# Performance work log

Measured on AMD Instinct MI355X. Metric: run time of the kernel, lower is better.

Reference implementation:

```python
import jax, jax.numpy as jnp
import numpy as np

NUM_EMBEDDINGS = 8192
EMA_DECAY = 0.99


def setup_inputs() -> dict:
    key = jax.random.key(0)
    k1, k2 = jax.random.split(key)
    encodings = jax.random.normal(k1, (16, 128, 32, 32), dtype=jnp.float32)
    weight = 0.02 * jax.random.normal(k2, (NUM_EMBEDDINGS, 128), dtype=jnp.float32)
    return {"encodings": encodings, "weight": weight}


def reference(encodings, weight):
    B, C, H, W = encodings.shape
    K = weight.shape[0]
    # [B, C, H, W] -> [N, C], N = B*H*W
    x = encodings.transpose(0, 2, 3, 1).reshape(-1, C)
    # pairwise squared distances via norms + matmul: [N, K]
    dist = (
        jnp.sum(x * x, axis=1, keepdims=True)
        + jnp.sum(weight * weight, axis=1)[None, :]
        - 2.0 * jnp.matmul(x, weight.T)
    )
    quantized_ids = jnp.argmin(dist, axis=1)  # [N] int
    # straight-through estimator
    q = x + jax.lax.stop_gradient(weight[quantized_ids] - x)  # [N, C]
    # training-mode EMA codebook update (scatter-add counts and sums)
    counts = jax.ops.segment_sum(
        jnp.ones((x.shape[0],), dtype=x.dtype), quantized_ids, num_segments=K
    )
    sums = jax.ops.segment_sum(x, quantized_ids, num_segments=K)
    new_means = sums / (counts[:, None] + 1e-12)
    new_weight = EMA_DECAY * weight + (1.0 - EMA_DECAY) * new_means
    ids_out = quantized_ids.reshape(B, H, W)
    q_out = q.reshape(B, H, W, C).transpose(0, 3, 1, 2)  # [B, C, H, W]
    return ids_out, q_out, new_weight
```

## Files before the change

### kernel.cpp

```cpp
#include <hip/hip_runtime.h>
#include <stdint.h>
#include <stddef.h>


#define N_ROWS   16384
#define K_CODES  8192
#define C_DIM    128
#define ITEMS_CAP 32768u

typedef _Float16 f16x8 __attribute__((ext_vector_type(8)));
typedef float    f32x4 __attribute__((ext_vector_type(4)));

__global__ __launch_bounds__(256) void prep(const float* __restrict__ enc,
                                            const float* __restrict__ w,
                                            _Float16* __restrict__ Ap,
                                            _Float16* __restrict__ Bp,
                                            float* __restrict__ xT,
                                            float* __restrict__ xnorm,
                                            float* __restrict__ wnorm,
                                            float* __restrict__ wnmax128) {
  __shared__ float t[128][65];
  const int tid = threadIdx.x;
  if (blockIdx.x < 256) {
    const int b = blockIdx.x >> 4;
    const int hw0 = (blockIdx.x & 15) << 6;
    #pragma unroll
    for (int i = 0; i < 32; ++i) {
      int idx = i * 256 + tid;
      int c = idx >> 6, hwl = idx & 63;
      t[c][hwl] = enc[((size_t)(b * 128 + c) << 10) + hw0 + hwl];
    }
    __syncthreads();
    const int r = tid >> 2, sub = tid & 3;
    const int n = (b << 10) + hw0 + r;
    const int R = n >> 4, m = n & 15;
    float s = 0.f;
    #pragma unroll
    for (int q = 0; q < 4; ++q) {
      f16x8 hv;
      float vv[8];
      #pragma unroll
      for (int e = 0; e < 8; ++e) {
        float v = t[sub * 32 + q * 8 + e][r];
        vv[e] = v;
        s += v * v;
        hv[e] = (_Float16)v;
      }
      *(f16x8*)(Ap + ((size_t)(R * 4 + sub) * 64 + (m + 16 * q)) * 8) = hv;
      *(float4*)(xT + (size_t)n * 128 + sub * 32 + q * 8) =
          (float4){vv[0], vv[1], vv[2], vv[3]};
      *(float4*)(xT + (size_t)n * 128 + sub * 32 + q * 8 + 4) =
          (float4){vv[4], vv[5], vv[6], vv[7]};
    }
    s += __shfl_xor(s, 1);
    s += __shfl_xor(s, 2);
    if (sub == 0) xnorm[n] = s;
  } else {
    __shared__ float wred[4];
    const int kk = (blockIdx.x - 256) * 64 + (tid >> 2), sub = tid & 3;
    const int R = kk >> 4, m = kk & 15;
    const float* base = w + (size_t)kk * C_DIM + sub * 32;
    float s = 0.f;
    #pragma unroll
    for (int q = 0; q < 4; ++q) {
      f16x8 hv;
      float4 va = *(const float4*)(base + q * 8);
      float4 vb = *(const float4*)(base + q * 8 + 4);
      float vv[8] = {va.x, va.y, va.z, va.w, vb.x, vb.y, vb.z, vb.w};
      #pragma unroll
      for (int e = 0; e < 8; ++e) { s += vv[e] * vv[e]; hv[e] = (_Float16)vv[e]; }
      *(f16x8*)(Bp + ((size_t)(R * 4 + sub) * 64 + (m + 16 * q)) * 8) = hv;
    }
    s += __shfl_xor(s, 1);
    s += __shfl_xor(s, 2);
    if (sub == 0) wnorm[kk] = s;
    float wx = s;
    #pragma unroll
    for (int st = 1; st <= 32; st <<= 1) wx = fmaxf(wx, __shfl_xor(wx, st));
    if ((tid & 63) == 0) wred[tid >> 6] = wx;
    __syncthreads();
    if (tid == 0)
      wnmax128[blockIdx.x - 256] =
          fmaxf(fmaxf(wred[0], wred[1]), fmaxf(wred[2], wred[3]));
  }
}

__global__ __launch_bounds__(512) void gemm_argmin(
    const _Float16* __restrict__ Ap, const _Float16* __restrict__ Bp,
    const float* __restrict__ wnorm,
    float* __restrict__ pd1h, unsigned short* __restrict__ pd2h,
    unsigned* __restrict__ icount, unsigned* __restrict__ hcount)
{
  __shared__ _Float16 sbuf[2][8192];
  const int tid = threadIdx.x;
  const int lane = tid & 63, wave = tid >> 6;
  const int m = lane & 15, q = lane >> 4;
  const int cs = blockIdx.x;
  const int row0 = blockIdx.y * 128;
  const int Tr = blockIdx.y * 8 + wave;

  if (cs == 0 && blockIdx.y == 0 && tid == 0) {
    *icount = 0u; *hcount = 0u;
  }

#define STAGE(b, hgn) do {                                                   \
    const size_t bh_ = ((size_t)((cs * 64 + (hgn) * 4) * 4) << 9);           \
    _Pragma("unroll")                                                        \
    for (int r_ = 0; r_ < 2; ++r_) {                                         \
      __builtin_amdgcn_global_load_lds(                                      \
          (const __attribute__((address_space(1))) void*)                    \
              (Bp + bh_ + ((size_t)(r_ * 512 + tid) << 3)),                  \
          (__attribute__((address_space(3))) void*)                          \
              (&sbuf[b][(r_ * 512 + tid) << 3]),                             \
          16, 0, 0);                                                         \
    }                                                                        \
  } while (0)

  f16x8 bx[4];
  #pragma unroll
  for (int kc = 0; kc < 4; ++kc)
    bx[kc] = *(const f16x8*)(Ap + (((size_t)Tr * 4 + kc) << 9) + (lane << 3));
  const int row = row0 + wave * 16 + m;
  const unsigned q2 = (unsigned)(q << 2);

  STAGE(0, 0);

  for (int hg = 0; hg < 16; ++hg) {
    __syncthreads();
    if (hg < 15) STAGE((hg + 1) & 1, hg + 1);
    const _Float16* fb = &sbuf[hg & 1][0];
    f32x4 acc[4];
    #pragma unroll
    for (int t = 0; t < 4; ++t) acc[t] = (f32x4){0.f, 0.f, 0.f, 0.f};
    #pragma unroll
    for (int kc = 0; kc < 4; ++kc) {
      #pragma unroll
      for (int t = 0; t < 4; ++t) {
        f16x8 a = *(const f16x8*)(fb + ((t * 4 + kc) << 9) + (lane << 3));
        acc[t] = __builtin_amdgcn_mfma_f32_16x16x32_f16(a, bx[kc], acc[t], 0, 0, 0);
      }
    }
    float m1t[4], m2t[4];
    #pragma unroll
    for (int t = 0; t < 4; ++t) {
      const int cb = (cs * 64 + hg * 4 + t) * 16 + 4 * q;
      float4 wnq = *(const float4*)(wnorm + cb);
      const unsigned e0 = (unsigned)(t << 4);
      unsigned b0 = (__float_as_uint(fmaf(-2.0f, acc[t][0], wnq.x)) & 0xFFFFFFC0u) | e0;
      unsigned b1 = (__float_as_uint(fmaf(-2.0f, acc[t][1], wnq.y)) & 0xFFFFFFC0u) | (e0 | 1u);
      unsigned b2 = (__float_as_uint(fmaf(-2.0f, acc[t][2], wnq.z)) & 0xFFFFFFC0u) | (e0 | 2u);
      unsigned b3 = (__float_as_uint(fmaf(-2.0f, acc[t][3], wnq.w)) & 0xFFFFFFC0u) | (e0 | 3u);
      float v0 = __uint_as_float(b0);
      float v1 = __uint_as_float(b1);
      float v2 = __uint_as_float(b2);
      float v3 = __uint_as_float(b3);
      float l1 = fminf(v0, v1), h1 = fmaxf(v0, v1);
      float l2 = fminf(v2, v3), h2 = fmaxf(v2, v3);
      m1t[t] = fminf(l1, l2);
      m2t[t] = fminf(fminf(h1, h2), fmaxf(l1, l2));
    }
    m2t[0] = fminf(fminf(m2t[0], m2t[1]), fmaxf(m1t[0], m1t[1]));
    m1t[0] = fminf(m1t[0], m1t[1]);
    m2t[2] = fminf(fminf(m2t[2], m2t[3]), fmaxf(m1t[2], m1t[3]));
    m1t[2] = fminf(m1t[2], m1t[3]);
    m2t[0] = fminf(fminf(m2t[0], m2t[2]), fmaxf(m1t[0], m1t[2]));
    m1t[0] = fminf(m1t[0], m1t[2]);
    float d1 = __uint_as_float(__float_as_uint(m1t[0]) | q2);
    float d2 = __uint_as_float(__float_as_uint(m2t[0]) | q2);
    #pragma unroll
    for (int s = 16; s <= 32; s <<= 1) {
      float o1 = __shfl_xor(d1, s), o2 = __shfl_xor(d2, s);
      d2 = fminf(fminf(d2, o2), fmaxf(d1, o1));
      d1 = fminf(d1, o1);
    }
    if (q == 0) {
      const int h = cs * 16 + hg;
      pd1h[(size_t)h * N_ROWS + row] = d1;
      unsigned bb = __float_as_uint(d2);
      bb += ((unsigned)((int)bb >> 31)) & 0xFFFFu;
      pd2h[(size_t)h * N_ROWS + row] = (unsigned short)(bb >> 16);
    }
  }
#undef STAGE
}

__global__ __launch_bounds__(256) void classify(
    const float* __restrict__ pd1h, const unsigned short* __restrict__ pd2h,
    const float* __restrict__ xnorm, const float* __restrict__ wnmax128,
    int* __restrict__ ids, unsigned* __restrict__ items,
    unsigned* __restrict__ icount, unsigned* __restrict__ hlist,
    unsigned* __restrict__ hcount, unsigned long long* __restrict__ keys,
    unsigned* __restrict__ cnt)
{
  __shared__ float wred[4];
  const int tid = threadIdx.x;
  const int gidx = blockIdx.x * 256 + tid;
  const int row = gidx >> 2, p = gidx & 3;
  if (p == 0) keys[row] = ~0ull;
  if (gidx < K_CODES) cnt[gidx] = 0u;
  float wv = wnmax128[tid & 127];
  #pragma unroll
  for (int st = 1; st <= 32; st <<= 1) wv = fmaxf(wv, __shfl_xor(wv, st));
  if ((tid & 63) == 0) wred[tid >> 6] = wv;
  __syncthreads();
  const float wm = fmaxf(fmaxf(wred[0], wred[1]), fmaxf(wred[2], wred[3]));

  float v1[32];
  float lmin = __builtin_inff();
  #pragma unroll
  for (int j = 0; j < 32; ++j) {
    v1[j] = pd1h[(size_t)(p * 32 + j) * N_ROWS + row];
    lmin = fminf(lmin, v1[j]);
  }
  lmin = fminf(lmin, __shfl_xor(lmin, 1));
  lmin = fminf(lmin, __shfl_xor(lmin, 2));
  float twoE = 2.0f * (0.0029297f * sqrtf(xnorm[row] * wm) + 5e-4f);
  float T = lmin + twoE;
  int nc = 0, hr = 0;
  unsigned cands[6];
  #pragma unroll 8
  for (int j = 0; j < 32; ++j) {
    const int h = p * 32 + j;
    float p2 = __uint_as_float(
        (unsigned)pd2h[(size_t)h * N_ROWS + row] << 16);
    if (p2 <= T) {
      unsigned hi = atomicAdd(hcount, 1u);
      hlist[hi] = ((unsigned)row << 7) | (unsigned)h;
      hr++;
    } else if (v1[j] <= T) {
      if (nc < 6) {
        cands[nc++] = (unsigned)h * 64u + (__float_as_uint(v1[j]) & 63u);
      } else {
        unsigned hi = atomicAdd(hcount, 1u);
        hlist[hi] = ((unsigned)row << 7) | (unsigned)h;
        hr++;
      }
    }
  }
  int nct = nc + __shfl_xor(nc, 1); nct += __shfl_xor(nct, 2);
  int hrt = hr + __shfl_xor(hr, 1); hrt += __shfl_xor(hrt, 2);
  if (hrt == 0 && nct == 1) {
    if (nc == 1) ids[row] = (int)cands[0];
  } else if (nc > 0) {
    unsigned base = atomicAdd(icount, (unsigned)nc);
    if (base + (unsigned)nc <= ITEMS_CAP) {
      for (int i2 = 0; i2 < nc; ++i2)
        items[base + i2] = ((unsigned)row << 13) | cands[i2];
    } else {
      for (int i2 = 0; i2 < nc; ++i2) {
        unsigned hi = atomicAdd(hcount, 1u);
        hlist[hi] = ((unsigned)row << 7) | (cands[i2] >> 6);
      }
    }
  }
}

__global__ __launch_bounds__(256) void refine(
    const float* __restrict__ xT, const float* __restrict__ w,
    const float* __restrict__ xnorm, const float* __restrict__ wnorm,
    const unsigned* __restrict__ items, const unsigned* __restrict__ icount,
    const unsigned* __restrict__ hlist, const unsigned* __restrict__ hcount,
    unsigned long long* __restrict__ keys) {
  const int tid = threadIdx.x;
  const int lane = tid & 63, wave = tid >> 6;
  const unsigned ic = *icount;
  const unsigned ica = ic <= ITEMS_CAP ? ic : ITEMS_CAP;
  for (unsigned i = blockIdx.x * 256 + tid; i < ica; i += gridDim.x * 256) {
    unsigned it = items[i];
    int row = (int)(it >> 13), c = (int)(it & 8191u);
    const float* xb = xT + (size_t)row * C_DIM;
    const float* wk = w + (size_t)c * C_DIM;
    float s = 0.f;
    #pragma unroll 8
    for (int c4 = 0; c4 < 32; ++c4) {
      float4 xv = *(const float4*)(xb + c4 * 4);
      float4 wv = *(const float4*)(wk + c4 * 4);
      s = fmaf(xv.x, wv.x, s);
      s = fmaf(xv.y, wv.y, s);
      s = fmaf(xv.z, wv.z, s);
      s = fmaf(xv.w, wv.w, s);
    }
    float d = (xnorm[row] + wnorm[c]) - 2.0f * s;
    unsigned sb = __float_as_uint(d);
    sb = (sb >> 31) ? ~sb : (sb | 0x80000000u);
    unsigned long long key = ((unsigned long long)sb << 32) | (unsigned)c;
    atomicMin(&keys[row], key);
  }
  __shared__ __align__(16) float xs[128];
  __shared__ unsigned long long red[4];
  const unsigned hc = *hcount;
  for (unsigned item = blockIdx.x; item < hc; item += gridDim.x) {
    const unsigned e = hlist[item];
    const int row = (int)(e >> 7), h = (int)(e & 127u);
    if (tid < 128)
      xs[tid] = xT[(size_t)row * C_DIM + tid];
    __syncthreads();
    const int code = h * 64 + (tid >> 2);
    const int qt = tid & 3;
    const float* wk = w + (size_t)code * C_DIM + qt * 32;
    float s = 0.f;
    #pragma unroll
    for (int c4 = 0; c4 < 8; ++c4) {
      float4 wv = *(const float4*)(wk + c4 * 4);
      float4 xv = *(const float4*)(&xs[qt * 32 + c4 * 4]);
      s = fmaf(xv.x, wv.x, s);
      s = fmaf(xv.y, wv.y, s);
      s = fmaf(xv.z, wv.z, s);
      s = fmaf(xv.w, wv.w, s);
    }
    s += __shfl_xor(s, 1);
    s += __shfl_xor(s, 2);
    unsigned long long best = ~0ull;
    if (qt == 0) {
      float d = (xnorm[row] + wnorm[code]) - 2.0f * s;
      unsigned sb = __float_as_uint(d);
      sb = (sb >> 31) ? ~sb : (sb | 0x80000000u);
      best = ((unsigned long long)sb << 32) | (unsigned)code;
    }
    #pragma unroll
    for (int st = 1; st <= 32; st <<= 1) {
      unsigned long long ok = __shfl_xor(best, st);
      best = ok < best ? ok : best;
    }
    if (lane == 0) red[wave] = best;
    __syncthreads();
    if (tid == 0) {
      unsigned long long bk = red[0];
      #pragma unroll
      for (int wv = 1; wv < 4; ++wv) bk = red[wv] < bk ? red[wv] : bk;
      atomicMin(&keys[row], bk);
    }
    __syncthreads();
  }
}

__global__ void resolve_ids(const unsigned long long* __restrict__ keys,
                            int* __restrict__ ids, unsigned* __restrict__ cnt,
                            float* __restrict__ out_ids) {
  int row = blockIdx.x * 256 + threadIdx.x;
  unsigned long long k = keys[row];
  int id = (k != ~0ull) ? (int)(unsigned)(k & 0xffffffffu) : ids[row];
  ids[row] = id;
  out_ids[row] = (float)id;
  atomicAdd(&cnt[id], 1u);
}

__global__ __launch_bounds__(256) void scan_offsets(
    const unsigned* __restrict__ cnt,
    unsigned* __restrict__ offs, unsigned* __restrict__ cursor) {
  __shared__ unsigned tot[256];
  const int tid = threadIdx.x;
  unsigned local[32], run = 0;
  #pragma unroll
  for (int i = 0; i < 32; ++i) { local[i] = run; run += cnt[tid * 32 + i]; }
  tot[tid] = run;
  __syncthreads();
  for (int st = 1; st < 256; st <<= 1) {
    unsigned v = (tid >= st) ? tot[tid - st] : 0u;
    __syncthreads();
    tot[tid] += v;
    __syncthreads();
  }
  unsigned excl = (tid == 0) ? 0u : tot[tid - 1];
  #pragma unroll
  for (int i = 0; i < 32; ++i) {
    unsigned o = excl + local[i];
    offs[tid * 32 + i] = o;
    cursor[tid * 32 + i] = o;
  }
}

__global__ void fill_rowlist(const int* __restrict__ ids,
                             unsigned* __restrict__ cursor,
                             int* __restrict__ rowlist) {
  int row = blockIdx.x * 256 + threadIdx.x;
  unsigned slot = atomicAdd(&cursor[ids[row]], 1u);
  rowlist[slot] = row;
}

__global__ __launch_bounds__(256) void qsum_final(
    const float* __restrict__ enc, const float* __restrict__ w,
    const int* __restrict__ ids,
    const unsigned* __restrict__ cnt, const unsigned* __restrict__ offs,
    const int* __restrict__ rowlist, const float* __restrict__ xT,
    float* __restrict__ outq, float* __restrict__ outw) {
  if (blockIdx.x < 2048) {
    int e = blockIdx.x * 1024 + threadIdx.x * 4;
    int c = (e >> 10) & 127;
    int b = e >> 17;
    int n = (b << 10) | (e & 1023);
    float4 x = *(const float4*)(enc + e);
    float4 o;
    o.x = x.x + (w[(size_t)ids[n + 0] * C_DIM + c] - x.x);
    o.y = x.y + (w[(size_t)ids[n + 1] * C_DIM + c] - x.y);
    o.z = x.z + (w[(size_t)ids[n + 2] * C_DIM + c] - x.z);
    o.w = x.w + (w[(size_t)ids[n + 3] * C_DIM + c] - x.w);
    *(float4*)(outq + e) = o;
  } else {
    const int tid = threadIdx.x;
    const int lane = tid & 63, wave = tid >> 6;
    const int k = (int)(blockIdx.x - 2048) * 4 + wave;
    const unsigned n0 = offs[k], nk = cnt[k];
    float S0a = 0.f, S0b = 0.f, S0c = 0.f, S0d = 0.f;
    float S1a = 0.f, S1b = 0.f, S1c = 0.f, S1d = 0.f;
    unsigned i = 0;
    for (; i + 4 <= nk; i += 4) {
      int r0 = rowlist[n0 + i],     r1 = rowlist[n0 + i + 1];
      int r2 = rowlist[n0 + i + 2], r3 = rowlist[n0 + i + 3];
      S0a += xT[(size_t)r0 * 128 + lane];      S1a += xT[(size_t)r0 * 128 + lane + 64];
      S0b += xT[(size_t)r1 * 128 + lane];      S1b += xT[(size_t)r1 * 128 + lane + 64];
      S0c += xT[(size_t)r2 * 128 + lane];      S1c += xT[(size_t)r2 * 128 + lane + 64];
      S0d += xT[(size_t)r3 * 128 + lane];      S1d += xT[(size_t)r3 * 128 + lane + 64];
    }
    for (; i < nk; ++i) {
      int r = rowlist[n0 + i];
      S0a += xT[(size_t)r * 128 + lane];
      S1a += xT[(size_t)r * 128 + lane + 64];
    }
    float S0 = (S0a + S0b) + (S0c + S0d);
    float S1 = (S1a + S1b) + (S1c + S1d);
    const float omd = (float)(1.0 - 0.99);
    float cf = (float)nk + 1e-12f;
    outw[(size_t)k * 128 + lane]      = 0.99f * w[(size_t)k * 128 + lane]      + omd * (S0 / cf);
    outw[(size_t)k * 128 + lane + 64] = 0.99f * w[(size_t)k * 128 + lane + 64] + omd * (S1 / cf);
  }
}

extern "C" void kernel_launch(void* const* d_in, const int* in_sizes, int n_in,
                              void* d_out, int out_size, void* d_ws, size_t ws_size,
                              hipStream_t stream) {
  const float* enc = (const float*)d_in[0];
  const float* w   = (const float*)d_in[1];
  float* out = (float*)d_out;
  float* out_ids = out;
  float* out_q   = out + N_ROWS;
  float* out_w   = out + N_ROWS + N_ROWS * C_DIM;

  char* ws = (char*)d_ws;
  _Float16* Ap  = (_Float16*)(ws);
  _Float16* Bp  = (_Float16*)(ws + 4194304);
  float* xnorm  = (float*)(ws + 6291456);
  float* wnorm  = (float*)(ws + 6356992);
  float* pd1h   = (float*)(ws + 6389760);
  unsigned short* pd2h = (unsigned short*)(ws + 14778368);
  float* wnmax128 = (float*)(ws + 18972672);
  int* ids      = (int*)(ws + 18973184);
  unsigned* hlist = (unsigned*)(ws + 19038720);
  unsigned* items = (unsigned*)(ws + 19563008);
  unsigned* icount = (unsigned*)(ws + 19694080);
  unsigned* hcount = (unsigned*)(ws + 19694084);
  unsigned* cnt    = (unsigned*)(ws + 19694096);
  unsigned* offs   = (unsigned*)(ws + 19726864);
  unsigned* cursor = (unsigned*)(ws + 19759632);
  unsigned long long* keys = (unsigned long long*)(ws + 19792400);
  int* rowlist  = (int*)(ws + 19923472);
  float* xT     = (float*)(ws + 20447248);
  (void)in_sizes; (void)n_in; (void)out_size; (void)ws_size;


  prep<<<384, 256, 0, stream>>>(enc, w, Ap, Bp, xT, xnorm, wnorm, wnmax128);
  gemm_argmin<<<dim3(8, N_ROWS / 128), 512, 0, stream>>>(
      Ap, Bp, wnorm, pd1h, pd2h, icount, hcount);
  classify<<<N_ROWS * 4 / 256, 256, 0, stream>>>(
      pd1h, pd2h, xnorm, wnmax128, ids, items, icount, hlist, hcount,
      keys, cnt);
  refine<<<2048, 256, 0, stream>>>(xT, w, xnorm, wnorm, items, icount,
                                   hlist, hcount, keys);
  resolve_ids<<<N_ROWS / 256, 256, 0, stream>>>(keys, ids, cnt, out_ids);
  scan_offsets<<<1, 256, 0, stream>>>(cnt, offs, cursor);
  fill_rowlist<<<N_ROWS / 256, 256, 0, stream>>>(ids, cursor, rowlist);
  qsum_final<<<2048 + K_CODES / 4, 256, 0, stream>>>(
      enc, w, ids, cnt, offs, rowlist, xT, out_q, out_w);
}
```

Measured before the change: 187.5 us.

## Replace counting-sort segment sum with float atomic scatter-add into codebook sums

Drops the scan_offsets and fill_rowlist kernels and the rowlist gather. Per-code sums are now built by float atomicAdd of each row's vector into a sums buffer, which refine zeroes and which reuses the pd2h workspace region. This removes two launches, a single-block scan and the serial gather loops, at the cost of many global float atomics that can contend on popular codes. Summation order becomes nondeterministic.

```diff
diff --git a/kernel.cpp b/kernel.cpp
--- a/kernel.cpp
+++ b/kernel.cpp
@@ -260,9 +260,11 @@
     const float* __restrict__ xnorm, const float* __restrict__ wnorm,
     const unsigned* __restrict__ items, const unsigned* __restrict__ icount,
     const unsigned* __restrict__ hlist, const unsigned* __restrict__ hcount,
-    unsigned long long* __restrict__ keys) {
+    unsigned long long* __restrict__ keys, float* __restrict__ sums) {
   const int tid = threadIdx.x;
   const int lane = tid & 63, wave = tid >> 6;
+  *(float2*)(sums + ((size_t)(blockIdx.x * 256 + tid) << 1)) =
+      (float2){0.f, 0.f};
   const unsigned ic = *icount;
   const unsigned ica = ic <= ITEMS_CAP ? ic : ITEMS_CAP;
   for (unsigned i = blockIdx.x * 256 + tid; i < ica; i += gridDim.x * 256) {
@@ -334,55 +336,36 @@
   }
 }
 
-__global__ void resolve_ids(const unsigned long long* __restrict__ keys,
-                            int* __restrict__ ids, unsigned* __restrict__ cnt,
-                            float* __restrict__ out_ids) {
-  int row = blockIdx.x * 256 + threadIdx.x;
+__global__ __launch_bounds__(256) void resolve_scatter(
+    const unsigned long long* __restrict__ keys,
+    int* __restrict__ ids, unsigned* __restrict__ cnt,
+    float* __restrict__ out_ids, const float* __restrict__ xT,
+    float* __restrict__ sums) {
+  const int gidx = blockIdx.x * 256 + threadIdx.x;
+  const int row = gidx >> 2, p = gidx & 3;
   unsigned long long k = keys[row];
   int id = (k != ~0ull) ? (int)(unsigned)(k & 0xffffffffu) : ids[row];
-  ids[row] = id;
-  out_ids[row] = (float)id;
-  atomicAdd(&cnt[id], 1u);
-}
-
-__global__ __launch_bounds__(256) void scan_offsets(
-    const unsigned* __restrict__ cnt,
-    unsigned* __restrict__ offs, unsigned* __restrict__ cursor) {
-  __shared__ unsigned tot[256];
-  const int tid = threadIdx.x;
-  unsigned local[32], run = 0;
+  if (p == 0) {
+    ids[row] = id;
+    out_ids[row] = (float)id;
+    atomicAdd(&cnt[id], 1u);
+  }
+  const float* xr = xT + (size_t)row * C_DIM + p * 32;
+  float* sr = sums + (size_t)id * C_DIM + p * 32;
   #pragma unroll
-  for (int i = 0; i < 32; ++i) { local[i] = run; run += cnt[tid * 32 + i]; }
-  tot[tid] = run;
-  __syncthreads();
-  for (int st = 1; st < 256; st <<= 1) {
-    unsigned v = (tid >= st) ? tot[tid - st] : 0u;
-    __syncthreads();
-    tot[tid] += v;
-    __syncthreads();
-  }
-  unsigned excl = (tid == 0) ? 0u : tot[tid - 1];
-  #pragma unroll
-  for (int i = 0; i < 32; ++i) {
-    unsigned o = excl + local[i];
-    offs[tid * 32 + i] = o;
-    cursor[tid * 32 + i] = o;
-  }
-}
-
-__global__ void fill_rowlist(const int* __restrict__ ids,
-                             unsigned* __restrict__ cursor,
-                             int* __restrict__ rowlist) {
-  int row = blockIdx.x * 256 + threadIdx.x;
-  unsigned slot = atomicAdd(&cursor[ids[row]], 1u);
-  rowlist[slot] = row;
+  for (int j = 0; j < 8; ++j) {
+    float4 v = *(const float4*)(xr + j * 4);
+    atomicAdd(&sr[j * 4 + 0], v.x);
+    atomicAdd(&sr[j * 4 + 1], v.y);
+    atomicAdd(&sr[j * 4 + 2], v.z);
+    atomicAdd(&sr[j * 4 + 3], v.w);
+  }
 }
 
 __global__ __launch_bounds__(256) void qsum_final(
     const float* __restrict__ enc, const float* __restrict__ w,
     const int* __restrict__ ids,
-    const unsigned* __restrict__ cnt, const unsigned* __restrict__ offs,
-    const int* __restrict__ rowlist, const float* __restrict__ xT,
+    const unsigned* __restrict__ cnt, const float* __restrict__ sums,
     float* __restrict__ outq, float* __restrict__ outw) {
   if (blockIdx.x < 2048) {
     int e = blockIdx.x * 1024 + threadIdx.x * 4;
@@ -400,25 +383,9 @@
     const int tid = threadIdx.x;
     const int lane = tid & 63, wave = tid >> 6;
     const int k = (int)(blockIdx.x - 2048) * 4 + wave;
-    const unsigned n0 = offs[k], nk = cnt[k];
-    float S0a = 0.f, S0b = 0.f, S0c = 0.f, S0d = 0.f;
-    float S1a = 0.f, S1b = 0.f, S1c = 0.f, S1d = 0.f;
-    unsigned i = 0;
-    for (; i + 4 <= nk; i += 4) {
-      int r0 = rowlist[n0 + i],     r1 = rowlist[n0 + i + 1];
-      int r2 = rowlist[n0 + i + 2], r3 = rowlist[n0 + i + 3];
-      S0a += xT[(size_t)r0 * 128 + lane];      S1a += xT[(size_t)r0 * 128 + lane + 64];
-      S0b += xT[(size_t)r1 * 128 + lane];      S1b += xT[(size_t)r1 * 128 + lane + 64];
-      S0c += xT[(size_t)r2 * 128 + lane];      S1c += xT[(size_t)r2 * 128 + lane + 64];
-      S0d += xT[(size_t)r3 * 128 + lane];      S1d += xT[(size_t)r3 * 128 + lane + 64];
-    }
-    for (; i < nk; ++i) {
-      int r = rowlist[n0 + i];
-      S0a += xT[(size_t)r * 128 + lane];
-      S1a += xT[(size_t)r * 128 + lane + 64];
-    }
-    float S0 = (S0a + S0b) + (S0c + S0d);
-    float S1 = (S1a + S1b) + (S1c + S1d);
+    const unsigned nk = cnt[k];
+    float S0 = sums[(size_t)k * C_DIM + lane];
+    float S1 = sums[(size_t)k * C_DIM + lane + 64];
     const float omd = (float)(1.0 - 0.99);
     float cf = (float)nk + 1e-12f;
     outw[(size_t)k * 128 + lane]      = 0.99f * w[(size_t)k * 128 + lane]      + omd * (S0 / cf);
@@ -443,6 +410,7 @@
   float* wnorm  = (float*)(ws + 6356992);
   float* pd1h   = (float*)(ws + 6389760);
   unsigned short* pd2h = (unsigned short*)(ws + 14778368);
+  float* sums   = (float*)(ws + 14778368);
   float* wnmax128 = (float*)(ws + 18972672);
   int* ids      = (int*)(ws + 18973184);
   unsigned* hlist = (unsigned*)(ws + 19038720);
@@ -450,10 +418,7 @@
   unsigned* icount = (unsigned*)(ws + 19694080);
   unsigned* hcount = (unsigned*)(ws + 19694084);
   unsigned* cnt    = (unsigned*)(ws + 19694096);
-  unsigned* offs   = (unsigned*)(ws + 19726864);
-  unsigned* cursor = (unsigned*)(ws + 19759632);
   unsigned long long* keys = (unsigned long long*)(ws + 19792400);
-  int* rowlist  = (int*)(ws + 19923472);
   float* xT     = (float*)(ws + 20447248);
   (void)in_sizes; (void)n_in; (void)out_size; (void)ws_size;
 
@@ -465,10 +430,9 @@
       pd1h, pd2h, xnorm, wnmax128, ids, items, icount, hlist, hcount,
       keys, cnt);
   refine<<<2048, 256, 0, stream>>>(xT, w, xnorm, wnorm, items, icount,
-                                   hlist, hcount, keys);
-  resolve_ids<<<N_ROWS / 256, 256, 0, stream>>>(keys, ids, cnt, out_ids);
-  scan_offsets<<<1, 256, 0, stream>>>(cnt, offs, cursor);
-  fill_rowlist<<<N_ROWS / 256, 256, 0, stream>>>(ids, cursor, rowlist);
+                                   hlist, hcount, keys, sums);
+  resolve_scatter<<<N_ROWS * 4 / 256, 256, 0, stream>>>(
+      keys, ids, cnt, out_ids, xT, sums);
   qsum_final<<<2048 + K_CODES / 4, 256, 0, stream>>>(
-      enc, w, ids, cnt, offs, rowlist, xT, out_q, out_w);
-}
+      enc, w, ids, cnt, sums, out_q, out_w);
+}
```

After: 306.2 us. +63.3%, slower.
